# Optimization experiments

Hardware: AMD Instinct MI355X
Metric: run time of the kernel (lower is better)

## Reference

```python
import jax, jax.numpy as jnp
import numpy as np

T, B, D = 2048, 16, 1024
SPECTRAL_RADIUS = 0.999
EPS = 1e-8
N_POWER_ITERS = 3


def _spectral_normalize(W, u):
    """Power iteration (no grad through u, v) then rescale W to spectral radius."""
    u0 = u / (jnp.linalg.norm(u) + EPS)
    v0 = jnp.zeros_like(u)

    def body(i, uv):
        uu, _ = uv
        vv = W.T @ uu
        vv = vv / (jnp.linalg.norm(vv) + EPS)
        uu = W @ vv
        uu = uu / (jnp.linalg.norm(uu) + EPS)
        return (uu, vv)

    uf, vf = jax.lax.fori_loop(0, N_POWER_ITERS, body, (u0, v0))
    uf = jax.lax.stop_gradient(uf)
    vf = jax.lax.stop_gradient(vf)
    sigma = jnp.abs(uf @ W @ vf)
    return W * (SPECTRAL_RADIUS / (sigma + EPS))


def setup_inputs() -> dict:
    key = jax.random.key(0)
    kx, kW, ku = jax.random.split(key, 3)
    xavier_std = float(np.sqrt(2.0 / (D + D)))  # ~0.0312
    return {
        "x": jax.random.normal(kx, (T, B, D), dtype=jnp.float32),
        "h0": jnp.zeros((B, D), dtype=jnp.float32),
        "W": jax.random.normal(kW, (D, D), dtype=jnp.float32) * xavier_std,
        "b": jnp.zeros((D,), dtype=jnp.float32),
        "u": jax.random.normal(ku, (D,), dtype=jnp.float32),
    }


def reference(x, h0, W, b, u):
    """h_t = Wn @ x_t + Wn @ h_{t-1} + b (tied, linear); output_t = h_t * silu(h_t).

    Returns (output [T,B,D], h [T+1,B,D]).
    """
    Wn = _spectral_normalize(W, u)
    # Precompute time-parallel part: Wn @ x_t + b for all t.
    Wx = jnp.einsum('tbd,ed->tbe', x, Wn) + b  # [T, B, D]

    def step(h_prev, wx_t):
        h_new = wx_t + h_prev @ Wn.T  # [B, D]
        return h_new, h_new

    _, hs = jax.lax.scan(step, h0, Wx)  # hs: [T, B, D]
    h = jnp.concatenate([h0[None], hs], axis=0)  # [T+1, B, D]
    output = hs * jax.nn.silu(hs)  # self-gating
    return output, h
```

## Files before the change

### kernel.cpp

```cpp
#include <hip/hip_runtime.h>
#include <math.h>

typedef unsigned short u16;
typedef __attribute__((ext_vector_type(8))) short short8;
typedef __attribute__((ext_vector_type(4))) float f32x4;

namespace {
constexpr int D = 1024;
constexpr int B = 16;
constexpr int T = 2048;
constexpr int L = 16;
constexpr int C = T / L;
constexpr float SR  = 0.999f;
constexpr float EPS = 1e-8f;
constexpr int SLICE = L * B * D;
constexpr int BD = B * D;
constexpr int UOFF = 131072;
constexpr int WOFF = 196608;
}

__device__ __forceinline__ u16 f2b(float f) {
  unsigned u = __float_as_uint(f);
  unsigned r = (u + 0x7fffu + ((u >> 16) & 1u)) >> 16;
  return (u16)r;
}
__device__ __forceinline__ float b2f(u16 v) {
  return __uint_as_float(((unsigned)v) << 16);
}

__device__ __forceinline__ short8 pack8(float4 a, float4 b) {
  short8 s;
  s[0] = (short)f2b(a.x); s[1] = (short)f2b(a.y);
  s[2] = (short)f2b(a.z); s[3] = (short)f2b(a.w);
  s[4] = (short)f2b(b.x); s[5] = (short)f2b(b.y);
  s[6] = (short)f2b(b.z); s[7] = (short)f2b(b.w);
  return s;
}


__global__ void mvT_kernel(const float* __restrict__ W, const float* __restrict__ vin,
                           float* __restrict__ vout) {
  int j = blockIdx.x * 256 + threadIdx.x;
  float acc = 0.f;
#pragma unroll 4
  for (int i = 0; i < D; ++i) acc += vin[i] * W[i * D + j];
  vout[j] = acc;
}

__global__ void mvN_kernel(const float* __restrict__ W, const float* __restrict__ vin,
                           float* __restrict__ vout) {
  __shared__ float red[256];
  int i = blockIdx.x, tid = threadIdx.x;
  float acc = 0.f;
  for (int j = tid; j < D; j += 256) acc += W[i * D + j] * vin[j];
  red[tid] = acc; __syncthreads();
  for (int s = 128; s > 0; s >>= 1) {
    if (tid < s) red[tid] += red[tid + s];
    __syncthreads();
  }
  if (tid == 0) vout[i] = red[0];
}

__global__ void scale_kernel(const float* __restrict__ t5, const float* __restrict__ t6,
                             float* __restrict__ scale_out) {
  __shared__ float r5[256], r6[256];
  int tid = threadIdx.x;
  float a5 = 0.f, a6 = 0.f;
  for (int i = tid; i < D; i += 256) { float x5 = t5[i], x6 = t6[i]; a5 += x5 * x5; a6 += x6 * x6; }
  r5[tid] = a5; r6[tid] = a6; __syncthreads();
  for (int s = 128; s > 0; s >>= 1) {
    if (tid < s) { r5[tid] += r5[tid + s]; r6[tid] += r6[tid + s]; }
    __syncthreads();
  }
  if (tid == 0) {
    float n5 = sqrtf(r5[0]), n6 = sqrtf(r6[0]);
    float sigma = n6 / (n5 + EPS);
    scale_out[0] = SR / (sigma + EPS);
  }
}

__global__ void cast_kernel(const float* __restrict__ W, const float* __restrict__ sc,
                            u16* __restrict__ WnB, u16* __restrict__ WnBT) {
  __shared__ float tile[32][33];
  float s = sc[0];
  int tx = threadIdx.x, ty = threadIdx.y;
  int bx = blockIdx.x, by = blockIdx.y;
#pragma unroll
  for (int k = 0; k < 4; ++k) {
    float v = W[(by * 32 + ty + 8 * k) * D + bx * 32 + tx];
    tile[ty + 8 * k][tx] = v;
    WnB[(by * 32 + ty + 8 * k) * D + bx * 32 + tx] = f2b(s * v);
  }
  __syncthreads();
#pragma unroll
  for (int k = 0; k < 4; ++k)
    WnBT[(bx * 32 + ty + 8 * k) * D + by * 32 + tx] = f2b(s * tile[tx][ty + 8 * k]);
}

__global__ __launch_bounds__(256)
void sqb_kernel(const u16* __restrict__ S, const u16* __restrict__ ST,
                u16* __restrict__ O, u16* __restrict__ OT) {
  const int tid = threadIdx.x;
  const int lane = tid & 63, wave = tid >> 6;
  const int lrow = lane & 15, quad = lane >> 4;
  const int m0 = blockIdx.y * 64;
  const int n0 = blockIdx.x * 64 + wave * 16;
  const short8* S8  = (const short8*)S;
  const short8* ST8 = (const short8*)ST;
  f32x4 acc[4];
#pragma unroll
  for (int i = 0; i < 4; ++i) acc[i] = (f32x4){0.f, 0.f, 0.f, 0.f};
  for (int kk = 0; kk < 32; ++kk) {
    short8 bfrag = ST8[(size_t)(n0 + lrow) * 128 + kk * 4 + quad];
#pragma unroll
    for (int mt = 0; mt < 4; ++mt) {
      short8 afrag = S8[(size_t)(m0 + mt * 16 + lrow) * 128 + kk * 4 + quad];
      acc[mt] = __builtin_amdgcn_mfma_f32_16x16x32_bf16(afrag, bfrag, acc[mt], 0, 0, 0);
    }
  }
#pragma unroll
  for (int mt = 0; mt < 4; ++mt)
#pragma unroll
    for (int r = 0; r < 4; ++r) {
      int m = m0 + mt * 16 + quad * 4 + r;
      int n = n0 + lrow;
      u16 v = f2b(acc[mt][r]);
      O[(size_t)m * D + n] = v;
      OT[(size_t)n * D + m] = v;
    }
}

__global__ void init_kernel(const float* __restrict__ h0, float* __restrict__ hbuf,
                            float* __restrict__ out, int* cnts, int* gens) {
  int i = blockIdx.x * 256 + threadIdx.x;
  float4 v = ((const float4*)h0)[i];
  ((float4*)hbuf)[i] = v;
  ((float4*)out)[i]  = v;
  if (i < 33) { cnts[i] = 0; gens[i] = 0; }
}


__device__ __forceinline__ void grid_bar(int* cnt, int* gen, int nblk) {
  __syncthreads();
  if (threadIdx.x == 0) {
    int g = __hip_atomic_load(gen, __ATOMIC_RELAXED, __HIP_MEMORY_SCOPE_AGENT);
    __threadfence();
    int prev = __hip_atomic_fetch_add(cnt, 1, __ATOMIC_RELAXED, __HIP_MEMORY_SCOPE_AGENT);
    if (prev == nblk - 1) {
      __hip_atomic_store(cnt, 0, __ATOMIC_RELAXED, __HIP_MEMORY_SCOPE_AGENT);
      __hip_atomic_store(gen, g + 1, __ATOMIC_RELEASE, __HIP_MEMORY_SCOPE_AGENT);
    } else {
      while (__hip_atomic_load(gen, __ATOMIC_RELAXED, __HIP_MEMORY_SCOPE_AGENT) == g)
        __builtin_amdgcn_s_sleep(2);
    }
    __builtin_amdgcn_fence(__ATOMIC_ACQUIRE, "agent");
  }
  __syncthreads();
}


__global__ __launch_bounds__(512, 2)
void phase1_kernel(const float* __restrict__ x, const u16* __restrict__ WnB,
                   const float* __restrict__ bias, float* __restrict__ hbuf,
                   int* cnts, int* gens) {
  __shared__ u16 Abuf[2][64 * 128];
  const int tid = threadIdx.x;
  const int lane = tid & 63, wave = tid >> 6;
  const int lrow = lane & 15, quad = lane >> 4;
  const int bid = blockIdx.x;
  const int mb = ((bid >> 6) << 3) | (bid & 7);
  const int nb = (bid >> 3) & 7;
  const int gr0 = mb * 64;
  const int nw = nb * 128 + wave * 16 + lrow;
  const short8* Wn8 = (const short8*)WnB;

  short8 bfrag[32];
#pragma unroll
  for (int kk = 0; kk < 32; ++kk)
    bfrag[kk] = Wn8[(size_t)nw * 128 + kk * 4 + quad];

  const float bcol = bias[nw];

  const int rr = tid >> 4;
  const int v_ = tid & 15;
  const int row0 = rr, row1 = 32 + rr;
  const int su0 = v_ ^ (row0 & 7), su1 = v_ ^ (row1 & 7);
  const int gra = gr0 + row0, grb = gr0 + row1;
  const int ca = gra >> 4, ba = gra & 15;
  const int cb = grb >> 4, bb = grb & 15;
  const size_t fa_base = (size_t)ba * 1024 + su0 * 8;
  const size_t fb_base = (size_t)bb * 1024 + su1 * 8;
  const int slot0 = row0 * 16 + v_, slot1 = row1 * 16 + v_;

  auto stage_load = [&](int sc, int j, short8& s0, short8& s1) {
    const size_t ta = (size_t)(ca * L + j - 1) * BD + fa_base + sc * 128;
    const size_t tb = (size_t)(cb * L + j - 1) * BD + fb_base + sc * 128;
    float4 x0 = ((const float4*)(x + ta))[0];
    float4 x1 = ((const float4*)(x + ta))[1];
    float4 y0 = ((const float4*)(x + tb))[0];
    float4 y1 = ((const float4*)(x + tb))[1];
    if (j > 1) {
      float4 h0v = ((const float4*)(hbuf + ta))[0];
      float4 h1v = ((const float4*)(hbuf + ta))[1];
      float4 h2v = ((const float4*)(hbuf + tb))[0];
      float4 h3v = ((const float4*)(hbuf + tb))[1];
      x0.x += h0v.x; x0.y += h0v.y; x0.z += h0v.z; x0.w += h0v.w;
      x1.x += h1v.x; x1.y += h1v.y; x1.z += h1v.z; x1.w += h1v.w;
      y0.x += h2v.x; y0.y += h2v.y; y0.z += h2v.z; y0.w += h2v.w;
      y1.x += h3v.x; y1.y += h3v.y; y1.z += h3v.z; y1.w += h3v.w;
    }
    s0 = pack8(x0, x1);
    s1 = pack8(y0, y1);
  };

  for (int j = 1; j <= L; ++j) {
    short8 s0, s1;
    stage_load(0, j, s0, s1);
    ((short8*)Abuf[0])[slot0] = s0;
    ((short8*)Abuf[0])[slot1] = s1;

    f32x4 acc[4];
#pragma unroll
    for (int mt = 0; mt < 4; ++mt) acc[mt] = (f32x4){bcol, bcol, bcol, bcol};

#pragma unroll
    for (int cc = 0; cc < 8; ++cc) {
      const int cur = cc & 1;
      if (cc < 7) stage_load(cc + 1, j, s0, s1);
      __syncthreads();
      const short8* A8 = (const short8*)Abuf[cur];
#pragma unroll
      for (int kp = 0; kp < 4; ++kp) {
#pragma unroll
        for (int mt = 0; mt < 4; ++mt) {
          short8 av = A8[(mt * 16 + lrow) * 16 + ((kp * 4 + quad) ^ (lrow & 7))];
          acc[mt] = __builtin_amdgcn_mfma_f32_16x16x32_bf16(av, bfrag[cc * 4 + kp], acc[mt], 0, 0, 0);
        }
      }
      if (cc < 7) {
        short8* Wd = (short8*)Abuf[cur ^ 1];
        Wd[slot0] = s0;
        Wd[slot1] = s1;
      }
    }

#pragma unroll
    for (int mt = 0; mt < 4; ++mt) {
#pragma unroll
      for (int r = 0; r < 4; ++r) {
        const int gr = gr0 + mt * 16 + quad * 4 + r;
        const int c = gr >> 4, b = gr & 15;
        hbuf[(size_t)(c * L + j) * BD + (size_t)b * 1024 + nw] = acc[mt][r];
      }
    }
    if (j < L) grid_bar(&cnts[mb], &gens[mb], 8);
  }
}


template<int NT>
__device__ __forceinline__ void load_state(const float* __restrict__ src,
                                           u16* Ghi, u16* Glo, int tid) {
  const float4* S4 = (const float4*)src;
  ushort4* H4 = (ushort4*)Ghi;
  ushort4* L4 = (ushort4*)Glo;
#pragma unroll
  for (int i = tid; i < 4096; i += NT) {
    float4 v = S4[i];
    ushort4 h, l;
    h.x = f2b(v.x); h.y = f2b(v.y); h.z = f2b(v.z); h.w = f2b(v.w);
    l.x = f2b(v.x - b2f(h.x)); l.y = f2b(v.y - b2f(h.y));
    l.z = f2b(v.z - b2f(h.z)); l.w = f2b(v.w - b2f(h.w));
    int si = i ^ (((i >> 8) & 7) << 1);
    H4[si] = h; L4[si] = l;
  }
}

__device__ __forceinline__ f32x4 state_matvec(const short8* Ghi8, const short8* Glo8,
                                              const short8* bfrag, int base, int swz) {
  f32x4 a0 = (f32x4){0.f, 0.f, 0.f, 0.f};
  f32x4 a1 = (f32x4){0.f, 0.f, 0.f, 0.f};
  f32x4 a2 = (f32x4){0.f, 0.f, 0.f, 0.f};
  f32x4 a3 = (f32x4){0.f, 0.f, 0.f, 0.f};
#pragma unroll
  for (int kk = 0; kk < 32; kk += 2) {
    int s0 = (base + kk * 4) ^ swz;
    int s1 = (base + kk * 4 + 4) ^ swz;
    a0 = __builtin_amdgcn_mfma_f32_16x16x32_bf16(Ghi8[s0], bfrag[kk],     a0, 0, 0, 0);
    a1 = __builtin_amdgcn_mfma_f32_16x16x32_bf16(Glo8[s0], bfrag[kk],     a1, 0, 0, 0);
    a2 = __builtin_amdgcn_mfma_f32_16x16x32_bf16(Ghi8[s1], bfrag[kk + 1], a2, 0, 0, 0);
    a3 = __builtin_amdgcn_mfma_f32_16x16x32_bf16(Glo8[s1], bfrag[kk + 1], a3, 0, 0, 0);
  }
  return (a0 + a1) + (a2 + a3);
}

__global__ __launch_bounds__(512, 2)
void p2a_kernel(const u16* __restrict__ A16, const float* __restrict__ hbuf,
                float* __restrict__ out, int* cnts, int* gens) {
  __shared__ u16 Ghi[16 * 1024];
  __shared__ u16 Glo[16 * 1024];
  const int tid = threadIdx.x;
  const int lane = tid & 63, wave = tid >> 6;
  const int lrow = lane & 15, quad = lane >> 4;
  const int g = blockIdx.x & 7, k = blockIdx.x >> 3;
  const int e = k * 128 + wave * 16 + lrow;
  const short8* A8   = (const short8*)A16;
  const short8* Ghi8 = (const short8*)Ghi;
  const short8* Glo8 = (const short8*)Glo;

  short8 bfrag[32];
#pragma unroll
  for (int kk = 0; kk < 32; ++kk)
    bfrag[kk] = A8[(size_t)e * 128 + kk * 4 + quad];

  {
    const float* v1 = hbuf + (size_t)(16 * g + 1) * SLICE;
    float* u1 = out + (size_t)(16 * g + 1) * SLICE + UOFF;
    for (int idx = tid; idx < 2048; idx += 512) {
      int b = idx >> 7, ee = k * 128 + (idx & 127);
      u1[b * 1024 + ee] = v1[b * 1024 + ee];
    }
    load_state<512>(v1, Ghi, Glo, tid);
  }

  const int jmax = (g == 7) ? 15 : 16;
  const int base = lrow * 128 + quad;
  const int swz = lrow & 7;
  for (int j = 2; j <= jmax; ++j) {
    const int c = 16 * g + j;
    float vl[4];
#pragma unroll
    for (int r = 0; r < 4; ++r)
      vl[r] = hbuf[(size_t)c * SLICE + (quad * 4 + r) * 1024 + e];
    __syncthreads();
    f32x4 acc = state_matvec(Ghi8, Glo8, bfrag, base, swz);
    float* ust = out + (size_t)c * SLICE + UOFF + e;
#pragma unroll
    for (int r = 0; r < 4; ++r) ust[(quad * 4 + r) * 1024] = acc[r] + vl[r];
    if (j < jmax) {
      grid_bar(&cnts[g], &gens[g], 8);
      load_state<512>(out + (size_t)c * SLICE + UOFF, Ghi, Glo, tid);
    }
  }
}

__global__ __launch_bounds__(256)
void p2b_kernel(const u16* __restrict__ A256, float* __restrict__ out,
                int* cnt, int* gen) {
  __shared__ u16 Ghi[16 * 1024];
  __shared__ u16 Glo[16 * 1024];
  const int tid = threadIdx.x;
  const int lane = tid & 63, wave = tid >> 6;
  const int lrow = lane & 15, quad = lane >> 4;
  const int e = (blockIdx.x * 4 + wave) * 16 + lrow;
  const short8* A8   = (const short8*)A256;
  const short8* Ghi8 = (const short8*)Ghi;
  const short8* Glo8 = (const short8*)Glo;

  short8 bfrag[32];
#pragma unroll
  for (int kk = 0; kk < 32; ++kk)
    bfrag[kk] = A8[(size_t)e * 128 + kk * 4 + quad];

  load_state<256>(out, Ghi, Glo, tid);

  float hl[4];
#pragma unroll
  for (int r = 0; r < 4; ++r)
    hl[r] = out[(size_t)16 * SLICE + UOFF + (quad * 4 + r) * 1024 + e];

  const int base = lrow * 128 + quad;
  const int swz = lrow & 7;
  for (int g = 0; g < 7; ++g) {
    __syncthreads();
    f32x4 acc = state_matvec(Ghi8, Glo8, bfrag, base, swz);
    float* orow = out + (size_t)(16 * (g + 1)) * SLICE + e;
#pragma unroll
    for (int r = 0; r < 4; ++r) orow[(quad * 4 + r) * 1024] = acc[r] + hl[r];
    if (g < 6) {
#pragma unroll
      for (int r = 0; r < 4; ++r)
        hl[r] = out[(size_t)(16 * (g + 2)) * SLICE + UOFF + (quad * 4 + r) * 1024 + e];
      grid_bar(cnt, gen, gridDim.x);
      load_state<256>(out + (size_t)(16 * (g + 1)) * SLICE, Ghi, Glo, tid);
    }
  }
}

__global__ __launch_bounds__(512, 2)
void p2c_kernel(const u16* __restrict__ A16, float* __restrict__ out,
                int* cnts, int* gens) {
  __shared__ u16 Ghi[16 * 1024];
  __shared__ u16 Glo[16 * 1024];
  const int tid = threadIdx.x;
  const int lane = tid & 63, wave = tid >> 6;
  const int lrow = lane & 15, quad = lane >> 4;
  const int g = blockIdx.x & 7, k = blockIdx.x >> 3;
  const int e = k * 128 + wave * 16 + lrow;
  const short8* A8   = (const short8*)A16;
  const short8* Ghi8 = (const short8*)Ghi;
  const short8* Glo8 = (const short8*)Glo;

  short8 bfrag[32];
#pragma unroll
  for (int kk = 0; kk < 32; ++kk)
    bfrag[kk] = A8[(size_t)e * 128 + kk * 4 + quad];

  load_state<512>(out + (size_t)(16 * g) * SLICE, Ghi, Glo, tid);

  const int base = lrow * 128 + quad;
  const int swz = lrow & 7;
  for (int j = 1; j <= 15; ++j) {
    const int c = 16 * g + j;
    float ul[4];
#pragma unroll
    for (int r = 0; r < 4; ++r)
      ul[r] = out[(size_t)c * SLICE + UOFF + (quad * 4 + r) * 1024 + e];
    __syncthreads();
    f32x4 acc = state_matvec(Ghi8, Glo8, bfrag, base, swz);
    float* srow = out + (size_t)c * SLICE + e;
#pragma unroll
    for (int r = 0; r < 4; ++r) srow[(quad * 4 + r) * 1024] = acc[r] + ul[r];
    if (j < 15) {
      float* wrow = out + (size_t)c * SLICE + WOFF + e;
#pragma unroll
      for (int r = 0; r < 4; ++r) wrow[(quad * 4 + r) * 1024] = acc[r];
      grid_bar(&cnts[g], &gens[g], 8);
      load_state<512>(out + (size_t)c * SLICE + WOFF, Ghi, Glo, tid);
    }
  }
}

__global__ void w0_kernel(const float* __restrict__ out, u16* __restrict__ Wping) {
  int i4 = blockIdx.x * 256 + threadIdx.x;
  int gr = i4 >> 8, du = i4 & 255;
  int c = gr >> 4, b = gr & 15;
  float4 v = ((const float4*)out)[(size_t)c * (SLICE / 4) + b * 256 + du];
  ushort4 g; g.x = f2b(v.x); g.y = f2b(v.y); g.z = f2b(v.z); g.w = f2b(v.w);
  ((ushort4*)Wping)[i4] = g;
}


__global__ __launch_bounds__(512, 2)
void phase3_kernel(const u16* __restrict__ WnB, float* __restrict__ hbuf,
                   float* __restrict__ out, u16* __restrict__ Wping,
                   u16* __restrict__ Wpong, int* cnts, int* gens) {
  __shared__ u16 Abuf[2][64 * 128];
  const int tid = threadIdx.x;
  const int lane = tid & 63, wave = tid >> 6;
  const int lrow = lane & 15, quad = lane >> 4;
  const int bid = blockIdx.x;
  const int mb = ((bid >> 6) << 3) | (bid & 7);
  const int nb = (bid >> 3) & 7;
  const int gr0 = mb * 64;
  const int nw = nb * 128 + wave * 16 + lrow;
  const short8* Wn8 = (const short8*)WnB;

  short8 bfrag[32];
#pragma unroll
  for (int kk = 0; kk < 32; ++kk)
    bfrag[kk] = Wn8[(size_t)nw * 128 + kk * 4 + quad];

  const int rr = tid >> 4;
  const int v_ = tid & 15;
  const int row0 = rr, row1 = 32 + rr;
  const int su0 = v_ ^ (row0 & 7), su1 = v_ ^ (row1 & 7);
  const size_t gra = gr0 + row0, grb = gr0 + row1;
  const int slot0 = row0 * 16 + v_, slot1 = row1 * 16 + v_;

  for (int j = 1; j <= L; ++j) {
    const short8* Wsrc = (const short8*)((j & 1) ? Wping : Wpong);
    u16* Wdst = (j & 1) ? Wpong : Wping;

    short8 s0 = Wsrc[gra * 128 + 0 * 16 + su0];
    short8 s1 = Wsrc[grb * 128 + 0 * 16 + su1];
    ((short8*)Abuf[0])[slot0] = s0;
    ((short8*)Abuf[0])[slot1] = s1;

    f32x4 acc[4];
#pragma unroll
    for (int mt = 0; mt < 4; ++mt) acc[mt] = (f32x4){0.f, 0.f, 0.f, 0.f};

#pragma unroll
    for (int cc = 0; cc < 8; ++cc) {
      const int cur = cc & 1;
      if (cc < 7) {
        s0 = Wsrc[gra * 128 + (cc + 1) * 16 + su0];
        s1 = Wsrc[grb * 128 + (cc + 1) * 16 + su1];
      }
      __syncthreads();
      const short8* A8 = (const short8*)Abuf[cur];
#pragma unroll
      for (int kp = 0; kp < 4; ++kp) {
#pragma unroll
        for (int mt = 0; mt < 4; ++mt) {
          short8 av = A8[(mt * 16 + lrow) * 16 + ((kp * 4 + quad) ^ (lrow & 7))];
          acc[mt] = __builtin_amdgcn_mfma_f32_16x16x32_bf16(av, bfrag[cc * 4 + kp], acc[mt], 0, 0, 0);
        }
      }
      if (cc < 7) {
        short8* Wd = (short8*)Abuf[cur ^ 1];
        Wd[slot0] = s0;
        Wd[slot1] = s1;
      }
    }

#pragma unroll
    for (int mt = 0; mt < 4; ++mt) {
#pragma unroll
      for (int r = 0; r < 4; ++r) {
        const int gr = gr0 + mt * 16 + quad * 4 + r;
        const int c = gr >> 4, b = gr & 15;
        float wv = acc[mt][r];
        size_t off = (size_t)(c * L + j) * BD + (size_t)b * 1024 + nw;
        float hv = hbuf[off] + wv;
        hbuf[off] = hv;
        float o = hv * hv / (1.f + __expf(-hv));
        out[off - BD] = o;
        if (j < L) Wdst[(size_t)gr * 1024 + nw] = f2b(wv);
      }
    }
    if (j < L) grid_bar(&cnts[mb], &gens[mb], 8);
  }
}


extern "C" void kernel_launch(void* const* d_in, const int* in_sizes, int n_in,
                              void* d_out, int out_size, void* d_ws, size_t ws_size,
                              hipStream_t stream) {
  const float* x    = (const float*)d_in[0];
  const float* h0   = (const float*)d_in[1];
  const float* W    = (const float*)d_in[2];
  const float* bias = (const float*)d_in[3];
  const float* u    = (const float*)d_in[4];
  float* out  = (float*)d_out;
  float* hbuf = out + (size_t)T * B * D;

  char* wsb = (char*)d_ws;
  float* va = (float*)wsb;
  float* vb = (float*)(wsb + 4096);
  float* sc = (float*)(wsb + 8192);
  int* cnts = (int*)(wsb + 8192 + 64);
  int* gens = cnts + 33;
  u16* WnB  = (u16*)(wsb + 16384);
  u16* WnBT = WnB  + (size_t)D * D;
  u16* P1   = WnBT + (size_t)D * D;
  u16* P1T  = P1   + (size_t)D * D;
  u16* P2   = P1T  + (size_t)D * D;
  u16* P2T  = P2   + (size_t)D * D;
  u16* Q    = P2T  + (size_t)D * D;
  u16* QT   = Q    + (size_t)D * D;

  mvT_kernel<<<4, 256, 0, stream>>>(W, u, va);
  mvN_kernel<<<1024, 256, 0, stream>>>(W, va, vb);
  mvT_kernel<<<4, 256, 0, stream>>>(W, vb, va);
  mvN_kernel<<<1024, 256, 0, stream>>>(W, va, vb);
  mvT_kernel<<<4, 256, 0, stream>>>(W, vb, va);
  mvN_kernel<<<1024, 256, 0, stream>>>(W, va, vb);
  scale_kernel<<<1, 256, 0, stream>>>(va, vb, sc);

  cast_kernel<<<dim3(32, 32), dim3(32, 8), 0, stream>>>(W, sc, WnB, WnBT);

  sqb_kernel<<<dim3(16, 16), 256, 0, stream>>>(WnB, WnBT, P1, P1T);
  sqb_kernel<<<dim3(16, 16), 256, 0, stream>>>(P1, P1T, P2, P2T);
  sqb_kernel<<<dim3(16, 16), 256, 0, stream>>>(P2, P2T, P1, P1T);
  sqb_kernel<<<dim3(16, 16), 256, 0, stream>>>(P1, P1T, P2, P2T);
  sqb_kernel<<<dim3(16, 16), 256, 0, stream>>>(P2, P2T, P1, P1T);
  sqb_kernel<<<dim3(16, 16), 256, 0, stream>>>(P1, P1T, Q, QT);
  sqb_kernel<<<dim3(16, 16), 256, 0, stream>>>(Q, QT, P1, P1T);
  sqb_kernel<<<dim3(16, 16), 256, 0, stream>>>(P1, P1T, Q, QT);

  init_kernel<<<16, 256, 0, stream>>>(h0, hbuf, out, cnts, gens);

  phase1_kernel<<<256, 512, 0, stream>>>(x, WnB, bias, hbuf, cnts, gens);

  p2a_kernel<<<64, 512, 0, stream>>>(P2, hbuf, out, cnts, gens);
  p2b_kernel<<<16, 256, 0, stream>>>(Q, out, &cnts[32], &gens[32]);
  p2c_kernel<<<64, 512, 0, stream>>>(P2, out, cnts, gens);

  w0_kernel<<<2048, 256, 0, stream>>>(out, P1);

  phase3_kernel<<<256, 512, 0, stream>>>(WnB, hbuf, out, P1, P2, cnts, gens);
}
```

Measured before the change: 1.791 ms.

## Split phase1/phase3 into 64-column tiles with LDS-staged coalesced epilogue; fuse w0

Result: slower. 2.051 ms (+14.5%).

```diff
diff --git a/kernel.cpp b/kernel.cpp
--- a/kernel.cpp
+++ b/kernel.cpp
@@ -131,11 +131,14 @@
 }
 
 __global__ void init_kernel(const float* __restrict__ h0, float* __restrict__ hbuf,
-                            float* __restrict__ out, int* cnts, int* gens) {
+                            float* __restrict__ out, u16* __restrict__ Wping,
+                            int* cnts, int* gens) {
   int i = blockIdx.x * 256 + threadIdx.x;
   float4 v = ((const float4*)h0)[i];
   ((float4*)hbuf)[i] = v;
   ((float4*)out)[i]  = v;
+  ushort4 g4; g4.x = f2b(v.x); g4.y = f2b(v.y); g4.z = f2b(v.z); g4.w = f2b(v.w);
+  ((ushort4*)Wping)[i] = g4;
   if (i < 33) { cnts[i] = 0; gens[i] = 0; }
 }
 
@@ -158,52 +161,51 @@
   __syncthreads();
 }
 
-
-__global__ __launch_bounds__(512, 2)
+__global__ __launch_bounds__(256, 2)
 void phase1_kernel(const float* __restrict__ x, const u16* __restrict__ WnB,
                    const float* __restrict__ bias, float* __restrict__ hbuf,
                    int* cnts, int* gens) {
-  __shared__ u16 Abuf[2][64 * 128];
+  __shared__ union {
+    u16 a[2][64 * 64];
+    float e[64 * 68];
+  } S;
   const int tid = threadIdx.x;
   const int lane = tid & 63, wave = tid >> 6;
   const int lrow = lane & 15, quad = lane >> 4;
   const int bid = blockIdx.x;
-  const int mb = ((bid >> 6) << 3) | (bid & 7);
-  const int nb = (bid >> 3) & 7;
+  const int mb = (bid & 7) * 4 + ((bid >> 3) & 3);
+  const int nb = bid >> 5;
   const int gr0 = mb * 64;
-  const int nw = nb * 128 + wave * 16 + lrow;
+  const int n0 = nb * 64;
+  const int nw = n0 + wave * 16 + lrow;
   const short8* Wn8 = (const short8*)WnB;
 
   short8 bfrag[32];
 #pragma unroll
   for (int kk = 0; kk < 32; ++kk)
     bfrag[kk] = Wn8[(size_t)nw * 128 + kk * 4 + quad];
-
   const float bcol = bias[nw];
 
-  const int rr = tid >> 4;
-  const int v_ = tid & 15;
-  const int row0 = rr, row1 = 32 + rr;
+  const int v_ = tid & 7;
+  const int row0 = tid >> 3, row1 = row0 + 32;
   const int su0 = v_ ^ (row0 & 7), su1 = v_ ^ (row1 & 7);
+  const int slot0 = row0 * 8 + v_, slot1 = row1 * 8 + v_;
   const int gra = gr0 + row0, grb = gr0 + row1;
-  const int ca = gra >> 4, ba = gra & 15;
-  const int cb = grb >> 4, bb = grb & 15;
-  const size_t fa_base = (size_t)ba * 1024 + su0 * 8;
-  const size_t fb_base = (size_t)bb * 1024 + su1 * 8;
-  const int slot0 = row0 * 16 + v_, slot1 = row1 * 16 + v_;
-
-  auto stage_load = [&](int sc, int j, short8& s0, short8& s1) {
-    const size_t ta = (size_t)(ca * L + j - 1) * BD + fa_base + sc * 128;
-    const size_t tb = (size_t)(cb * L + j - 1) * BD + fb_base + sc * 128;
-    float4 x0 = ((const float4*)(x + ta))[0];
-    float4 x1 = ((const float4*)(x + ta))[1];
-    float4 y0 = ((const float4*)(x + tb))[0];
-    float4 y1 = ((const float4*)(x + tb))[1];
+  const size_t fa = (size_t)((gra >> 4) * L) * BD + (size_t)(gra & 15) * 1024 + su0 * 8;
+  const size_t fb = (size_t)((grb >> 4) * L) * BD + (size_t)(grb & 15) * 1024 + su1 * 8;
+
+  auto stage_load = [&](int cc, int j, short8& s0, short8& s1) {
+    const size_t oa = fa + (size_t)(j - 1) * BD + cc * 64;
+    const size_t ob = fb + (size_t)(j - 1) * BD + cc * 64;
+    float4 x0 = ((const float4*)(x + oa))[0];
+    float4 x1 = ((const float4*)(x + oa))[1];
+    float4 y0 = ((const float4*)(x + ob))[0];
+    float4 y1 = ((const float4*)(x + ob))[1];
     if (j > 1) {
-      float4 h0v = ((const float4*)(hbuf + ta))[0];
-      float4 h1v = ((const float4*)(hbuf + ta))[1];
-      float4 h2v = ((const float4*)(hbuf + tb))[0];
-      float4 h3v = ((const float4*)(hbuf + tb))[1];
+      float4 h0v = ((const float4*)(hbuf + oa))[0];
+      float4 h1v = ((const float4*)(hbuf + oa))[1];
+      float4 h2v = ((const float4*)(hbuf + ob))[0];
+      float4 h3v = ((const float4*)(hbuf + ob))[1];
       x0.x += h0v.x; x0.y += h0v.y; x0.z += h0v.z; x0.w += h0v.w;
       x1.x += h1v.x; x1.y += h1v.y; x1.z += h1v.z; x1.w += h1v.w;
       y0.x += h2v.x; y0.y += h2v.y; y0.z += h2v.z; y0.w += h2v.w;
@@ -216,44 +218,51 @@
   for (int j = 1; j <= L; ++j) {
     short8 s0, s1;
     stage_load(0, j, s0, s1);
-    ((short8*)Abuf[0])[slot0] = s0;
-    ((short8*)Abuf[0])[slot1] = s1;
+    ((short8*)S.a[0])[slot0] = s0;
+    ((short8*)S.a[0])[slot1] = s1;
 
     f32x4 acc[4];
 #pragma unroll
     for (int mt = 0; mt < 4; ++mt) acc[mt] = (f32x4){bcol, bcol, bcol, bcol};
 
 #pragma unroll
-    for (int cc = 0; cc < 8; ++cc) {
+    for (int cc = 0; cc < 16; ++cc) {
       const int cur = cc & 1;
-      if (cc < 7) stage_load(cc + 1, j, s0, s1);
+      if (cc < 15) stage_load(cc + 1, j, s0, s1);
       __syncthreads();
-      const short8* A8 = (const short8*)Abuf[cur];
-#pragma unroll
-      for (int kp = 0; kp < 4; ++kp) {
+      const short8* A8 = (const short8*)S.a[cur];
+#pragma unroll
+      for (int kp = 0; kp < 2; ++kp) {
 #pragma unroll
         for (int mt = 0; mt < 4; ++mt) {
-          short8 av = A8[(mt * 16 + lrow) * 16 + ((kp * 4 + quad) ^ (lrow & 7))];
-          acc[mt] = __builtin_amdgcn_mfma_f32_16x16x32_bf16(av, bfrag[cc * 4 + kp], acc[mt], 0, 0, 0);
+          short8 av = A8[(mt * 16 + lrow) * 8 + ((kp * 4 + quad) ^ (lrow & 7))];
+          acc[mt] = __builtin_amdgcn_mfma_f32_16x16x32_bf16(av, bfrag[cc * 2 + kp], acc[mt], 0, 0, 0);
         }
       }
-      if (cc < 7) {
-        short8* Wd = (short8*)Abuf[cur ^ 1];
-        Wd[slot0] = s0;
-        Wd[slot1] = s1;
+      if (cc < 15) {
+        ((short8*)S.a[cur ^ 1])[slot0] = s0;
+        ((short8*)S.a[cur ^ 1])[slot1] = s1;
       }
     }
 
-#pragma unroll
-    for (int mt = 0; mt < 4; ++mt) {
-#pragma unroll
-      for (int r = 0; r < 4; ++r) {
-        const int gr = gr0 + mt * 16 + quad * 4 + r;
-        const int c = gr >> 4, b = gr & 15;
-        hbuf[(size_t)(c * L + j) * BD + (size_t)b * 1024 + nw] = acc[mt][r];
-      }
-    }
-    if (j < L) grid_bar(&cnts[mb], &gens[mb], 8);
+    __syncthreads();
+#pragma unroll
+    for (int mt = 0; mt < 4; ++mt)
+#pragma unroll
+      for (int r = 0; r < 4; ++r)
+        S.e[(mt * 16 + quad * 4 + r) * 68 + wave * 16 + lrow] = acc[mt][r];
+    __syncthreads();
+
+#pragma unroll
+    for (int s = 0; s < 4; ++s) {
+      const int idx = tid + s * 256;
+      const int row = idx >> 4, f4 = idx & 15;
+      float4 v = *(const float4*)&S.e[row * 68 + f4 * 4];
+      const int gr = gr0 + row;
+      const size_t off = (size_t)((gr >> 4) * L + j) * BD + (size_t)(gr & 15) * 1024 + n0 + f4 * 4;
+      *(float4*)&hbuf[off] = v;
+    }
+    if (j < L) grid_bar(&cnts[mb], &gens[mb], 16);
   }
 }
 
@@ -346,7 +355,7 @@
 
 __global__ __launch_bounds__(256)
 void p2b_kernel(const u16* __restrict__ A256, float* __restrict__ out,
-                int* cnt, int* gen) {
+                u16* __restrict__ Wping, int* cnt, int* gen) {
   __shared__ u16 Ghi[16 * 1024];
   __shared__ u16 Glo[16 * 1024];
   const int tid = threadIdx.x;
@@ -374,22 +383,28 @@
   for (int g = 0; g < 7; ++g) {
     __syncthreads();
     f32x4 acc = state_matvec(Ghi8, Glo8, bfrag, base, swz);
-    float* orow = out + (size_t)(16 * (g + 1)) * SLICE + e;
-#pragma unroll
-    for (int r = 0; r < 4; ++r) orow[(quad * 4 + r) * 1024] = acc[r] + hl[r];
+    const int c1 = 16 * (g + 1);
+    float* orow = out + (size_t)c1 * SLICE + e;
+    u16* wrow = Wping + (size_t)(c1 * 16) * 1024 + e;
+#pragma unroll
+    for (int r = 0; r < 4; ++r) {
+      float sv = acc[r] + hl[r];
+      orow[(quad * 4 + r) * 1024] = sv;
+      wrow[(size_t)(quad * 4 + r) * 1024] = f2b(sv);
+    }
     if (g < 6) {
 #pragma unroll
       for (int r = 0; r < 4; ++r)
         hl[r] = out[(size_t)(16 * (g + 2)) * SLICE + UOFF + (quad * 4 + r) * 1024 + e];
       grid_bar(cnt, gen, gridDim.x);
-      load_state<256>(out + (size_t)(16 * (g + 1)) * SLICE, Ghi, Glo, tid);
+      load_state<256>(out + (size_t)c1 * SLICE, Ghi, Glo, tid);
     }
   }
 }
 
 __global__ __launch_bounds__(512, 2)
 void p2c_kernel(const u16* __restrict__ A16, float* __restrict__ out,
-                int* cnts, int* gens) {
+                u16* __restrict__ Wping, int* cnts, int* gens) {
   __shared__ u16 Ghi[16 * 1024];
   __shared__ u16 Glo[16 * 1024];
   const int tid = threadIdx.x;
@@ -419,41 +434,40 @@
     __syncthreads();
     f32x4 acc = state_matvec(Ghi8, Glo8, bfrag, base, swz);
     float* srow = out + (size_t)c * SLICE + e;
-#pragma unroll
-    for (int r = 0; r < 4; ++r) srow[(quad * 4 + r) * 1024] = acc[r] + ul[r];
+    u16* wrow = Wping + (size_t)(c * 16) * 1024 + e;
+#pragma unroll
+    for (int r = 0; r < 4; ++r) {
+      float sv = acc[r] + ul[r];
+      srow[(quad * 4 + r) * 1024] = sv;
+      wrow[(size_t)(quad * 4 + r) * 1024] = f2b(sv);
+    }
     if (j < 15) {
-      float* wrow = out + (size_t)c * SLICE + WOFF + e;
-#pragma unroll
-      for (int r = 0; r < 4; ++r) wrow[(quad * 4 + r) * 1024] = acc[r];
+      float* wst = out + (size_t)c * SLICE + WOFF + e;
+#pragma unroll
+      for (int r = 0; r < 4; ++r) wst[(quad * 4 + r) * 1024] = acc[r];
       grid_bar(&cnts[g], &gens[g], 8);
       load_state<512>(out + (size_t)c * SLICE + WOFF, Ghi, Glo, tid);
     }
   }
 }
 
-__global__ void w0_kernel(const float* __restrict__ out, u16* __restrict__ Wping) {
-  int i4 = blockIdx.x * 256 + threadIdx.x;
-  int gr = i4 >> 8, du = i4 & 255;
-  int c = gr >> 4, b = gr & 15;
-  float4 v = ((const float4*)out)[(size_t)c * (SLICE / 4) + b * 256 + du];
-  ushort4 g; g.x = f2b(v.x); g.y = f2b(v.y); g.z = f2b(v.z); g.w = f2b(v.w);
-  ((ushort4*)Wping)[i4] = g;
-}
-
-
-__global__ __launch_bounds__(512, 2)
+__global__ __launch_bounds__(256, 2)
 void phase3_kernel(const u16* __restrict__ WnB, float* __restrict__ hbuf,
                    float* __restrict__ out, u16* __restrict__ Wping,
                    u16* __restrict__ Wpong, int* cnts, int* gens) {
-  __shared__ u16 Abuf[2][64 * 128];
+  __shared__ union {
+    u16 a[2][64 * 64];
+    float e[64 * 68];
+  } S;
   const int tid = threadIdx.x;
   const int lane = tid & 63, wave = tid >> 6;
   const int lrow = lane & 15, quad = lane >> 4;
   const int bid = blockIdx.x;
-  const int mb = ((bid >> 6) << 3) | (bid & 7);
-  const int nb = (bid >> 3) & 7;
+  const int mb = (bid & 7) * 4 + ((bid >> 3) & 3);
+  const int nb = bid >> 5;
   const int gr0 = mb * 64;
-  const int nw = nb * 128 + wave * 16 + lrow;
+  const int n0 = nb * 64;
+  const int nw = n0 + wave * 16 + lrow;
   const short8* Wn8 = (const short8*)WnB;
 
   short8 bfrag[32];
@@ -461,66 +475,79 @@
   for (int kk = 0; kk < 32; ++kk)
     bfrag[kk] = Wn8[(size_t)nw * 128 + kk * 4 + quad];
 
-  const int rr = tid >> 4;
-  const int v_ = tid & 15;
-  const int row0 = rr, row1 = 32 + rr;
+  const int v_ = tid & 7;
+  const int row0 = tid >> 3, row1 = row0 + 32;
   const int su0 = v_ ^ (row0 & 7), su1 = v_ ^ (row1 & 7);
+  const int slot0 = row0 * 8 + v_, slot1 = row1 * 8 + v_;
   const size_t gra = gr0 + row0, grb = gr0 + row1;
-  const int slot0 = row0 * 16 + v_, slot1 = row1 * 16 + v_;
 
   for (int j = 1; j <= L; ++j) {
     const short8* Wsrc = (const short8*)((j & 1) ? Wping : Wpong);
     u16* Wdst = (j & 1) ? Wpong : Wping;
 
-    short8 s0 = Wsrc[gra * 128 + 0 * 16 + su0];
-    short8 s1 = Wsrc[grb * 128 + 0 * 16 + su1];
-    ((short8*)Abuf[0])[slot0] = s0;
-    ((short8*)Abuf[0])[slot1] = s1;
+    short8 s0 = Wsrc[gra * 128 + 0 * 8 + su0];
+    short8 s1 = Wsrc[grb * 128 + 0 * 8 + su1];
+    ((short8*)S.a[0])[slot0] = s0;
+    ((short8*)S.a[0])[slot1] = s1;
 
     f32x4 acc[4];
 #pragma unroll
     for (int mt = 0; mt < 4; ++mt) acc[mt] = (f32x4){0.f, 0.f, 0.f, 0.f};
 
 #pragma unroll
-    for (int cc = 0; cc < 8; ++cc) {
+    for (int cc = 0; cc < 16; ++cc) {
       const int cur = cc & 1;
-      if (cc < 7) {
-        s0 = Wsrc[gra * 128 + (cc + 1) * 16 + su0];
-        s1 = Wsrc[grb * 128 + (cc + 1) * 16 + su1];
+      if (cc < 15) {
+        s0 = Wsrc[gra * 128 + (cc + 1) * 8 + su0];
+        s1 = Wsrc[grb * 128 + (cc + 1) * 8 + su1];
       }
       __syncthreads();
-      const short8* A8 = (const short8*)Abuf[cur];
-#pragma unroll
-      for (int kp = 0; kp < 4; ++kp) {
+      const short8* A8 = (const short8*)S.a[cur];
+#pragma unroll
+      for (int kp = 0; kp < 2; ++kp) {
 #pragma unroll
         for (int mt = 0; mt < 4; ++mt) {
-          short8 av = A8[(mt * 16 + lrow) * 16 + ((kp * 4 + quad) ^ (lrow & 7))];
-          acc[mt] = __builtin_amdgcn_mfma_f32_16x16x32_bf16(av, bfrag[cc * 4 + kp], acc[mt], 0, 0, 0);
+          short8 av = A8[(mt * 16 + lrow) * 8 + ((kp * 4 + quad) ^ (lrow & 7))];
+          acc[mt] = __builtin_amdgcn_mfma_f32_16x16x32_bf16(av, bfrag[cc * 2 + kp], acc[mt], 0, 0, 0);
         }
       }
-      if (cc < 7) {
-        short8* Wd = (short8*)Abuf[cur ^ 1];
-        Wd[slot0] = s0;
-        Wd[slot1] = s1;
+      if (cc < 15) {
+        ((short8*)S.a[cur ^ 1])[slot0] = s0;
+        ((short8*)S.a[cur ^ 1])[slot1] = s1;
       }
     }
 
-#pragma unroll
-    for (int mt = 0; mt < 4; ++mt) {
-#pragma unroll
-      for (int r = 0; r < 4; ++r) {
-        const int gr = gr0 + mt * 16 + quad * 4 + r;
-        const int c = gr >> 4, b = gr & 15;
-        float wv = acc[mt][r];
-        size_t off = (size_t)(c * L + j) * BD + (size_t)b * 1024 + nw;
-        float hv = hbuf[off] + wv;
-        hbuf[off] = hv;
-        float o = hv * hv / (1.f + __expf(-hv));
-        out[off - BD] = o;
-        if (j < L) Wdst[(size_t)gr * 1024 + nw] = f2b(wv);
+    __syncthreads();
+#pragma unroll
+    for (int mt = 0; mt < 4; ++mt)
+#pragma unroll
+      for (int r = 0; r < 4; ++r)
+        S.e[(mt * 16 + quad * 4 + r) * 68 + wave * 16 + lrow] = acc[mt][r];
+    __syncthreads();
+
+#pragma unroll
+    for (int s = 0; s < 4; ++s) {
+      const int idx = tid + s * 256;
+      const int row = idx >> 4, f4 = idx & 15;
+      float4 wv = *(const float4*)&S.e[row * 68 + f4 * 4];
+      const int gr = gr0 + row;
+      const size_t off = (size_t)((gr >> 4) * L + j) * BD + (size_t)(gr & 15) * 1024 + n0 + f4 * 4;
+      float4 hv = *(const float4*)&hbuf[off];
+      hv.x += wv.x; hv.y += wv.y; hv.z += wv.z; hv.w += wv.w;
+      *(float4*)&hbuf[off] = hv;
+      float4 o;
+      o.x = hv.x * hv.x / (1.f + __expf(-hv.x));
+      o.y = hv.y * hv.y / (1.f + __expf(-hv.y));
+      o.z = hv.z * hv.z / (1.f + __expf(-hv.z));
+      o.w = hv.w * hv.w / (1.f + __expf(-hv.w));
+      *(float4*)&out[off - BD] = o;
+      if (j < L) {
+        ushort4 wb;
+        wb.x = f2b(wv.x); wb.y = f2b(wv.y); wb.z = f2b(wv.z); wb.w = f2b(wv.w);
+        *(ushort4*)&Wdst[(size_t)gr * 1024 + n0 + f4 * 4] = wb;
       }
     }
-    if (j < L) grid_bar(&cnts[mb], &gens[mb], 8);
+    if (j < L) grid_bar(&cnts[mb], &gens[mb], 16);
   }
 }
 
@@ -570,15 +597,13 @@
   sqb_kernel<<<dim3(16, 16), 256, 0, stream>>>(Q, QT, P1, P1T);
   sqb_kernel<<<dim3(16, 16), 256, 0, stream>>>(P1, P1T, Q, QT);
 
-  init_kernel<<<16, 256, 0, stream>>>(h0, hbuf, out, cnts, gens);
-
-  phase1_kernel<<<256, 512, 0, stream>>>(x, WnB, bias, hbuf, cnts, gens);
+  init_kernel<<<16, 256, 0, stream>>>(h0, hbuf, out, P1, cnts, gens);
+
+  phase1_kernel<<<512, 256, 0, stream>>>(x, WnB, bias, hbuf, cnts, gens);
 
   p2a_kernel<<<64, 512, 0, stream>>>(P2, hbuf, out, cnts, gens);
-  p2b_kernel<<<16, 256, 0, stream>>>(Q, out, &cnts[32], &gens[32]);
-  p2c_kernel<<<64, 512, 0, stream>>>(P2, out, cnts, gens);
-
-  w0_kernel<<<2048, 256, 0, stream>>>(out, P1);
-
-  phase3_kernel<<<256, 512, 0, stream>>>(WnB, hbuf, out, P1, P2, cnts, gens);
-}
+  p2b_kernel<<<16, 256, 0, stream>>>(Q, out, P1, &cnts[32], &gens[32]);
+  p2c_kernel<<<64, 512, 0, stream>>>(P2, out, P1, cnts, gens);
+
+  phase3_kernel<<<512, 256, 0, stream>>>(WnB, hbuf, out, P1, P2, cnts, gens);
+}
```
